# Optimization experiments

Hardware: AMD Instinct MI355X
Metric: run time of the kernel (lower is better)

Reference implementation:

```python
import jax, jax.numpy as jnp
import numpy as np

N = 50000      # nodes per type
E = 200000     # edges per relation
H, D = 4, 64   # heads, per-head dim
C = H * D      # hidden = hc_graph * heads = 256
L = 3          # num_hops (HGTConv layers)
HC_LIN, HC_TASK = 256, 128
OUT_DIMS = (3, 3, 3, 5, 1, 1, 8)  # ptr_l1/l2/l3, leaf_category, signed, floating, size


def setup_inputs() -> dict:
    key = jax.random.key(0)
    ks = jax.random.split(key, 24)
    f = lambda k, s: jax.random.normal(k, s, dtype=jnp.float32) * 0.05
    ri = lambda k: jax.random.randint(k, (E,), 0, N, dtype=jnp.int32)
    return {
        "xe": f(ks[0], (N, C)),
        "xs": f(ks[1], (N, C)),
        "ee_src": ri(ks[2]), "ee_dst": ri(ks[3]),
        "es_src": ri(ks[4]), "es_dst": ri(ks[5]),
        "se_src": ri(ks[6]), "se_dst": ri(ks[7]),
        # per-layer, per-node-type projections (2 node types)
        "Wk": f(ks[8], (L, 2, C, C)),
        "Wq": f(ks[9], (L, 2, C, C)),
        "Wv": f(ks[10], (L, 2, C, C)),
        "Wa": f(ks[11], (L, 2, C, C)),
        "skip": jnp.ones((L, 2), dtype=jnp.float32),
        # per-layer, per-relation attention/message transforms (3 relations)
        "Arel": f(ks[12], (L, 3, H, D, D)),
        "Mrel": f(ks[13], (L, 3, H, D, D)),
        "mu": jnp.ones((L, 3, H), dtype=jnp.float32),
        # shared linear stack + 7 task heads (final out padded to 8, sliced per head)
        "Wsh": f(ks[14], (2, HC_LIN, HC_LIN)),
        "bsh": jnp.zeros((2, HC_LIN), dtype=jnp.float32),
        "Wt1": f(ks[15], (7, HC_LIN, HC_TASK)),
        "bt1": jnp.zeros((7, HC_TASK), dtype=jnp.float32),
        "Wt2": f(ks[16], (7, HC_TASK, 8)),
        "bt2": jnp.zeros((7, 8), dtype=jnp.float32),
    }


def _seg_softmax(scores, seg, n):
    m = jax.ops.segment_max(scores, seg, num_segments=n)
    e = jnp.exp(scores - m[seg])
    s = jax.ops.segment_sum(e, seg, num_segments=n)
    return e / (s[seg] + 1e-16)


def _hgt_forward(xe, xs, ee_src, ee_dst, es_src, es_dst, se_src, se_dst,
                 Wk, Wq, Wv, Wa, skip, Arel, Mrel, mu, Wsh, bsh, Wt1, bt1, Wt2, bt2):
    inv_sqrt_d = 1.0 / jnp.sqrt(jnp.float32(D))

    def rel(k_src, v_src, q_dst, src, dst, A, M, m):
        kt = jnp.einsum('ehd,hdf->ehf', k_src[src], A)          # [E,H,D]
        score = (q_dst[dst] * kt).sum(-1) * (m * inv_sqrt_d)    # [E,H]
        msg = jnp.einsum('ehd,hdf->ehf', v_src[src], M)         # [E,H,D]
        return score, msg

    for l in range(L):
        ke = (xe @ Wk[l, 0]).reshape(N, H, D)
        qe = (xe @ Wq[l, 0]).reshape(N, H, D)
        ve = (xe @ Wv[l, 0]).reshape(N, H, D)
        ks_ = (xs @ Wk[l, 1]).reshape(N, H, D)
        qs = (xs @ Wq[l, 1]).reshape(N, H, D)
        vs = (xs @ Wv[l, 1]).reshape(N, H, D)

        s0, m0 = rel(ke, ve, qe, ee_src, ee_dst, Arel[l, 0], Mrel[l, 0], mu[l, 0])  # expr->expr
        s1, m1 = rel(ke, ve, qs, es_src, es_dst, Arel[l, 1], Mrel[l, 1], mu[l, 1])  # expr->stmt
        s2, m2 = rel(ks_, vs, qe, se_src, se_dst, Arel[l, 2], Mrel[l, 2], mu[l, 2])  # stmt->expr

        # destination 'expr': softmax over all incoming edges (rel0 + rel2)
        sc_e = jnp.concatenate([s0, s2], axis=0)
        ms_e = jnp.concatenate([m0, m2], axis=0)
        dst_e = jnp.concatenate([ee_dst, se_dst], axis=0)
        a_e = _seg_softmax(sc_e, dst_e, N)
        agg_e = jax.ops.segment_sum(a_e[..., None] * ms_e, dst_e, num_segments=N).reshape(N, C)

        # destination 'stmt': only rel1
        a_s = _seg_softmax(s1, es_dst, N)
        agg_s = jax.ops.segment_sum(a_s[..., None] * m1, es_dst, num_segments=N).reshape(N, C)

        be = jax.nn.sigmoid(skip[l, 0])
        bs = jax.nn.sigmoid(skip[l, 1])
        xe = be * (jax.nn.gelu(agg_e, approximate=False) @ Wa[l, 0]) + (1.0 - be) * xe
        xs = bs * (jax.nn.gelu(agg_s, approximate=False) @ Wa[l, 1]) + (1.0 - bs) * xs

    # shared linear stack on 'expr' nodes
    h = xe
    for i in range(Wsh.shape[0]):
        h = jax.nn.relu(h @ Wsh[i] + bsh[i])

    # 7 task heads: hidden layer + final (padded to 8 outputs, sliced per head)
    t = jax.nn.relu(jnp.einsum('nc,kct->knt', h, Wt1) + bt1[:, None, :])  # [7,N,HC_TASK]
    o = jnp.einsum('knt,kto->kno', t, Wt2) + bt2[:, None, :]              # [7,N,8]
    outs = [o[i, :, :d] for i, d in enumerate(OUT_DIMS)]
    return jnp.concatenate(outs, axis=-1)  # [N, 24]


def reference(xe, xs, ee_src, ee_dst, es_src, es_dst, se_src, se_dst,
              Wk, Wq, Wv, Wa, skip, Arel, Mrel, mu, Wsh, bsh, Wt1, bt1, Wt2, bt2):
    return _hgt_forward(xe, xs, ee_src, ee_dst, es_src, es_dst, se_src, se_dst,
                        Wk, Wq, Wv, Wa, skip, Arel, Mrel, mu, Wsh, bsh, Wt1, bt1, Wt2, bt2)
```

## Files before the change

### kernel.cpp

```cpp
#include <hip/hip_runtime.h>
#include <hip/hip_fp16.h>
#include <cmath>


#define CDIM 256
#define AR_R (256 * 256)

using f16x8 = __attribute__((ext_vector_type(8))) _Float16;
using f16x4 = __attribute__((ext_vector_type(4))) _Float16;
using f16x2 = __attribute__((ext_vector_type(2))) _Float16;
using f32x4 = __attribute__((ext_vector_type(4))) float;

__device__ __forceinline__ float gelu_f(float x) {
    return 0.5f * x * (1.0f + erff(x * 0.70710678118654752f));
}

__device__ __forceinline__ float dot8f(const f16x8 a, const f16x8 b, float r) {
#if __has_builtin(__builtin_amdgcn_fdot2)
#pragma unroll
    for (int t = 0; t < 4; ++t) {
        f16x2 av = {a[2 * t], a[2 * t + 1]};
        f16x2 bv = {b[2 * t], b[2 * t + 1]};
        r = __builtin_amdgcn_fdot2(av, bv, r, false);
    }
#else
#pragma unroll
    for (int t = 0; t < 8; ++t) r += (float)a[t] * (float)b[t];
#endif
    return r;
}

__global__ __launch_bounds__(256) void zero_k(int* __restrict__ p, size_t n) {
    size_t i = (size_t)blockIdx.x * blockDim.x + threadIdx.x;
    const size_t stride = (size_t)gridDim.x * blockDim.x;
    for (; i < n; i += stride) p[i] = 0;
}

__global__ __launch_bounds__(256) void cvt2_k(const float* __restrict__ xe_in,
                                              const float* __restrict__ xs_in,
                                              _Float16* __restrict__ xeH,
                                              _Float16* __restrict__ xsH,
                                              size_t n4) {
    const float* in = blockIdx.y ? xs_in : xe_in;
    _Float16* out = blockIdx.y ? xsH : xeH;
    size_t i = (size_t)blockIdx.x * blockDim.x + threadIdx.x;
    const size_t stride = (size_t)gridDim.x * blockDim.x;
    for (; i < n4; i += stride) {
        const float4 v = ((const float4*)in)[i];
        f16x4 o;
        o[0] = (_Float16)v.x; o[1] = (_Float16)v.y;
        o[2] = (_Float16)v.z; o[3] = (_Float16)v.w;
        ((f16x4*)out)[i] = o;
    }
}

__device__ __forceinline__ void cvtT_dev(const float* __restrict__ W,
                                         _Float16* __restrict__ dst) {
    const int o = blockIdx.x, c = threadIdx.x;
    dst[(size_t)o * 256 + c] = (_Float16)W[(size_t)c * 256 + o];
}

__device__ __forceinline__ void foldT_dev(const float* __restrict__ Wbase,
                                          const float* __restrict__ T,
                                          _Float16* __restrict__ dst) {
    __shared__ float row[256];
    const int c = blockIdx.x, t = threadIdx.x;
    row[t] = Wbase[(size_t)c * 256 + t];
    __syncthreads();
    const int h = t >> 6, f = t & 63;
    const float* Th = T + h * 4096;
    float acc = 0.f;
#pragma unroll 8
    for (int d = 0; d < 64; ++d) acc += row[h * 64 + d] * Th[d * 64 + f];
    dst[(size_t)t * 256 + c] = (_Float16)acc;
}

__global__ __launch_bounds__(256) void prep_layer_k(
    const float* __restrict__ Wk, const float* __restrict__ Wq,
    const float* __restrict__ Wv, const float* __restrict__ Wa,
    const float* __restrict__ Arel, const float* __restrict__ Mrel,
    _Float16* __restrict__ arena) {
    const size_t CC = 65536, HDD = 16384;
    const int l = blockIdx.y / 10;
    const int c = blockIdx.y % 10;
    _Float16* L = arena + (size_t)l * 10 * AR_R;
    const float* Wk0 = Wk + (l * 2 + 0) * CC;
    const float* Wk1 = Wk + (l * 2 + 1) * CC;
    const float* Wv0 = Wv + (l * 2 + 0) * CC;
    const float* Wv1 = Wv + (l * 2 + 1) * CC;
    switch (c) {
        case 0: cvtT_dev(Wq + (l * 2 + 0) * CC, L); break;
        case 1: foldT_dev(Wk0, Arel + (l * 3 + 0) * HDD, L + 1 * AR_R); break;
        case 2: foldT_dev(Wk0, Arel + (l * 3 + 1) * HDD, L + 2 * AR_R); break;
        case 3: cvtT_dev(Wq + (l * 2 + 1) * CC, L + 3 * AR_R); break;
        case 4: foldT_dev(Wk1, Arel + (l * 3 + 2) * HDD, L + 4 * AR_R); break;
        case 5: foldT_dev(Wv0, Mrel + (l * 3 + 0) * HDD, L + 5 * AR_R); break;
        case 6: foldT_dev(Wv0, Mrel + (l * 3 + 1) * HDD, L + 6 * AR_R); break;
        case 7: foldT_dev(Wv1, Mrel + (l * 3 + 2) * HDD, L + 7 * AR_R); break;
        case 8: cvtT_dev(Wa + (l * 2 + 0) * CC, L + 8 * AR_R); break;
        case 9: cvtT_dev(Wa + (l * 2 + 1) * CC, L + 9 * AR_R); break;
    }
}

__global__ __launch_bounds__(256) void prep_stack_k(const float* __restrict__ Wsh,
                                                    _Float16* __restrict__ SA) {
    cvtT_dev(Wsh + (size_t)blockIdx.y * 65536, SA + (size_t)blockIdx.y * AR_R);
}

__global__ __launch_bounds__(256) void prep_heads_k(const float* __restrict__ Wt1,
                                                    _Float16* __restrict__ HA) {
    const int o = blockIdx.x, k = blockIdx.y, c = threadIdx.x;
    HA[(size_t)(k * 128 + o) * 256 + c] =
        (_Float16)Wt1[(size_t)k * 256 * 128 + (size_t)c * 128 + o];
}

template <int EPI, bool SPLIT>
__device__ __forceinline__ void gemm_body(
    const _Float16* __restrict__ A, const _Float16* __restrict__ Bt,
    _Float16* __restrict__ C, int M, int Nc, int bm, int bn, size_t bufStride,
    const float* __restrict__ bias, const float* __restrict__ skipv,
    _Float16* As, _Float16* Bs) {
    const int tid = threadIdx.x;
    const int wave = tid >> 6, lane = tid & 63;
    const int wm = (wave >> 1) * 64, wn = (wave & 1) * 64;
    const int l15 = lane & 15, g = lane >> 4;

    f32x4 acc[4][4] = {};

    for (int k0 = 0; k0 < 256; k0 += 64) {
        __syncthreads();
#pragma unroll
        for (int p = 0; p < 4; ++p) {
            const int slot = p * 256 + tid;
            const int r = slot >> 3;
            const int cb = ((slot & 7) << 4) ^ ((r & 7) << 4);
            int gr = bm + r; if (gr >= M) gr = M - 1;
            __builtin_amdgcn_global_load_lds(
                (const __attribute__((address_space(1))) void*)
                    ((const char*)A + ((size_t)gr * 256 + k0) * 2 + cb),
                (__attribute__((address_space(3))) void*)((char*)As + slot * 16),
                16, 0, 0);
            __builtin_amdgcn_global_load_lds(
                (const __attribute__((address_space(1))) void*)
                    ((const char*)Bt + ((size_t)(bn + r) * 256 + k0) * 2 + cb),
                (__attribute__((address_space(3))) void*)((char*)Bs + slot * 16),
                16, 0, 0);
        }
        __syncthreads();
#pragma unroll
        for (int sub = 0; sub < 2; ++sub) {
            f16x8 af[4], bf[4];
#pragma unroll
            for (int i = 0; i < 4; ++i) {
                const int ra = wm + i * 16 + l15;
                const int rb = wn + i * 16 + l15;
                const int ka = (sub * 64 + g * 16) ^ ((ra & 7) << 4);
                const int kb = (sub * 64 + g * 16) ^ ((rb & 7) << 4);
                af[i] = *(const f16x8*)((const char*)As + ra * 128 + ka);
                bf[i] = *(const f16x8*)((const char*)Bs + rb * 128 + kb);
            }
#pragma unroll
            for (int mi = 0; mi < 4; ++mi)
#pragma unroll
                for (int ni = 0; ni < 4; ++ni)
                    acc[mi][ni] = __builtin_amdgcn_mfma_f32_16x16x32_f16(
                        af[mi], bf[ni], acc[mi][ni], 0, 0, 0);
        }
    }

    float be = 0.f, ombe = 0.f;
    if (EPI == 1) {
        const float s = skipv[0];
        be = 1.0f / (1.0f + expf(-s));
        ombe = 1.0f - be;
    }
#pragma unroll
    for (int mi = 0; mi < 4; ++mi) {
#pragma unroll
        for (int r = 0; r < 4; ++r) {
            const int row = bm + wm + mi * 16 + g * 4 + r;
            if (row >= M) continue;
#pragma unroll
            for (int ni = 0; ni < 4; ++ni) {
                const int colg = bn + wn + ni * 16 + l15;
                float v = acc[mi][ni][r];
                size_t idx;
                if (SPLIT)
                    idx = (size_t)(colg >> 8) * bufStride + (size_t)row * 256 +
                          (colg & 255);
                else
                    idx = (size_t)row * Nc + colg;
                if (EPI == 1) v = be * v + ombe * (float)C[idx];
                if (EPI == 2) v = fmaxf(v + bias[colg], 0.f);
                C[idx] = (_Float16)v;
            }
        }
    }
}

template <int EPI, bool SPLIT>
__global__ __launch_bounds__(256) void gemm_h(
    const _Float16* __restrict__ A, const _Float16* __restrict__ Bt,
    _Float16* __restrict__ C, int M, int Nc, size_t bufStride,
    const float* __restrict__ bias, const float* __restrict__ skipv) {
    __shared__ _Float16 As[128 * 64];
    __shared__ _Float16 Bs[128 * 64];
    gemm_body<EPI, SPLIT>(A, Bt, C, M, Nc, blockIdx.y * 128, blockIdx.x * 128,
                          bufStride, bias, skipv, As, Bs);
}

__global__ __launch_bounds__(256) void projq_k(
    const _Float16* __restrict__ xeH, const _Float16* __restrict__ xsH,
    const _Float16* __restrict__ L, _Float16* __restrict__ Hb, int M) {
    __shared__ _Float16 As[128 * 64];
    __shared__ _Float16 Bs[128 * 64];
    const int job = blockIdx.x >> 1;
    const int bn = (blockIdx.x & 1) * 128;
    const _Float16* A = (job < 3) ? xeH : xsH;
    const _Float16* Bt = L + (size_t)job * AR_R;
    _Float16* C = Hb + (size_t)job * (size_t)M * 256;
    gemm_body<0, false>(A, Bt, C, M, 256, blockIdx.y * 128, bn, 0, nullptr,
                        nullptr, As, Bs);
}

__global__ __launch_bounds__(256) void projv_k(
    const _Float16* __restrict__ xeH, const _Float16* __restrict__ xsH,
    const _Float16* __restrict__ L, _Float16* __restrict__ Hb, int M) {
    __shared__ _Float16 As[128 * 64];
    __shared__ _Float16 Bs[128 * 64];
    const int job = blockIdx.x >> 1;
    const int bn = (blockIdx.x & 1) * 128;
    const _Float16* A = (job < 2) ? xeH : xsH;
    const _Float16* Bt = L + (size_t)(5 + job) * AR_R;
    const int dsti = (job == 0) ? 1 : (job == 1) ? 2 : 4;
    _Float16* C = Hb + (size_t)dsti * (size_t)M * 256;
    gemm_body<0, false>(A, Bt, C, M, 256, blockIdx.y * 128, bn, 0, nullptr,
                        nullptr, As, Bs);
}

__global__ __launch_bounds__(256) void update2_k(
    const _Float16* __restrict__ aggE, const _Float16* __restrict__ aggS,
    const _Float16* __restrict__ WaT0, const _Float16* __restrict__ WaT1,
    _Float16* __restrict__ xeH, _Float16* __restrict__ xsH,
    const float* __restrict__ skipb, int M) {
    __shared__ _Float16 As[128 * 64];
    __shared__ _Float16 Bs[128 * 64];
    const int sel = blockIdx.x >> 1;
    const int bn = (blockIdx.x & 1) * 128;
    const int bm = blockIdx.y * 128;
    if (sel == 0)
        gemm_body<1, false>(aggE, WaT0, xeH, M, 256, bm, bn, 0, nullptr, skipb,
                            As, Bs);
    else
        gemm_body<1, false>(aggS, WaT1, xsH, M, 256, bm, bn, 0, nullptr,
                            skipb + 1, As, Bs);
}

__global__ __launch_bounds__(256) void hist3_k(const int* __restrict__ d0,
                                               const int* __restrict__ d1,
                                               const int* __restrict__ d2,
                                               int* __restrict__ cnt, int N,
                                               int E) {
    const int i = blockIdx.x * 256 + threadIdx.x;
    if (i >= E) return;
    const int r = blockIdx.y;
    const int* d = r == 0 ? d0 : r == 1 ? d1 : d2;
    atomicAdd(&cnt[(size_t)r * N + d[i]], 1);
}

__global__ __launch_bounds__(256) void partial_k(const int* __restrict__ cnt,
                                                 int* __restrict__ partials,
                                                 int N, int PB) {
    const int r = blockIdx.y, b = blockIdx.x, tid = threadIdx.x;
    const int gi = b * 256 + tid;
    int v = (gi < N) ? cnt[(size_t)r * N + gi] : 0;
#pragma unroll
    for (int o = 1; o < 64; o <<= 1) v += __shfl_xor(v, o);
    __shared__ int ws[4];
    if ((tid & 63) == 0) ws[tid >> 6] = v;
    __syncthreads();
    if (tid == 0) partials[r * PB + b] = ws[0] + ws[1] + ws[2] + ws[3];
}

__global__ __launch_bounds__(256) void scanp_k(int* __restrict__ partials,
                                               int* __restrict__ rp, int N,
                                               int PB, int E) {
    __shared__ int lds[256];
    const int r = blockIdx.y, tid = threadIdx.x;
    const int v = (tid < PB) ? partials[r * PB + tid] : 0;
    lds[tid] = v;
    __syncthreads();
    int acc = v;
    for (int off = 1; off < 256; off <<= 1) {
        const int t = (tid >= off) ? lds[tid - off] : 0;
        __syncthreads();
        acc += t;
        lds[tid] = acc;
        __syncthreads();
    }
    if (tid < PB) partials[r * PB + tid] = acc - v;
    if (tid == 0) rp[(size_t)r * (N + 1) + N] = E;
}

__global__ __launch_bounds__(256) void rpwrite_k(const int* __restrict__ cnt,
                                                 const int* __restrict__ partials,
                                                 int* __restrict__ rp, int N,
                                                 int PB) {
    __shared__ int lds[256];
    const int r = blockIdx.y, b = blockIdx.x, tid = threadIdx.x;
    const int gi = b * 256 + tid;
    const int v = (gi < N) ? cnt[(size_t)r * N + gi] : 0;
    lds[tid] = v;
    __syncthreads();
    int acc = v;
    for (int off = 1; off < 256; off <<= 1) {
        const int t = (tid >= off) ? lds[tid - off] : 0;
        __syncthreads();
        acc += t;
        lds[tid] = acc;
        __syncthreads();
    }
    if (gi < N) rp[(size_t)r * (N + 1) + gi] = partials[r * PB + b] + acc - v;
}

__global__ __launch_bounds__(256) void scatter3_k(
    const int* __restrict__ d0, const int* __restrict__ d1,
    const int* __restrict__ d2, const int* __restrict__ s0_,
    const int* __restrict__ s1_, const int* __restrict__ s2_,
    const int* __restrict__ rp, int* __restrict__ fill,
    int* __restrict__ colsrc, int N, int E) {
    const int i = blockIdx.x * 256 + threadIdx.x;
    if (i >= E) return;
    const int r = blockIdx.y;
    const int* d = r == 0 ? d0 : r == 1 ? d1 : d2;
    const int* s = r == 0 ? s0_ : r == 1 ? s1_ : s2_;
    const int dd = d[i];
    const int p = rp[(size_t)r * (N + 1) + dd] + atomicAdd(&fill[(size_t)r * N + dd], 1);
    colsrc[(size_t)r * E + p] = s[i];
}

__device__ __forceinline__ void score_rel_g(
    const f16x8 q0, const f16x8 q1, const _Float16* __restrict__ kA,
    const int* __restrict__ cs, int beg, int end, float scl,
    float* __restrict__ sc, int grp, int j, float& m) {
    int i = beg + grp;
    for (; i + 4 < end; i += 8) {
        const int sA = cs[i], sB = cs[i + 4];
        const _Float16* rowA = &kA[(size_t)sA * 256 + j * 16];
        const _Float16* rowB = &kA[(size_t)sB * 256 + j * 16];
        const f16x8 a0 = *(const f16x8*)rowA;
        const f16x8 a1 = *(const f16x8*)(rowA + 8);
        const f16x8 b0 = *(const f16x8*)rowB;
        const f16x8 b1 = *(const f16x8*)(rowB + 8);
        float p0 = dot8f(q1, a1, dot8f(q0, a0, 0.f));
        float p1 = dot8f(q1, b1, dot8f(q0, b0, 0.f));
        p0 += __shfl_xor(p0, 1); p1 += __shfl_xor(p1, 1);
        p0 += __shfl_xor(p0, 2); p1 += __shfl_xor(p1, 2);
        const float v0 = p0 * scl, v1 = p1 * scl;
        if ((j & 3) == 0) {
            sc[(size_t)i * 4 + (j >> 2)] = v0;
            sc[(size_t)(i + 4) * 4 + (j >> 2)] = v1;
            m = fmaxf(m, fmaxf(v0, v1));
        }
    }
    if (i < end) {
        const int sA = cs[i];
        const _Float16* row = &kA[(size_t)sA * 256 + j * 16];
        const f16x8 k0 = *(const f16x8*)row;
        const f16x8 k1 = *(const f16x8*)(row + 8);
        float p = dot8f(q1, k1, dot8f(q0, k0, 0.f));
        p += __shfl_xor(p, 1);
        p += __shfl_xor(p, 2);
        const float v = p * scl;
        if ((j & 3) == 0) {
            sc[(size_t)i * 4 + (j >> 2)] = v;
            m = fmaxf(m, v);
        }
    }
}

__global__ __launch_bounds__(256) void score3_k(
    const _Float16* __restrict__ qe, const _Float16* __restrict__ kA0,
    const _Float16* __restrict__ kA1, const _Float16* __restrict__ qs,
    const _Float16* __restrict__ kA2, const int* __restrict__ rp,
    const int* __restrict__ colsrc, const float* __restrict__ muL,
    float* __restrict__ sc, float* __restrict__ mx_e,
    float* __restrict__ mx_s, int N, int E) {
    const int wid = (blockIdx.x * blockDim.x + threadIdx.x) >> 6;
    if (wid >= N) return;
    const int lane = threadIdx.x & 63;
    const int grp = lane >> 4, j = lane & 15, h = j >> 2;
    const size_t E4 = (size_t)E * 4;
    float m = -1e30f;
    if (blockIdx.y == 0) {
        const _Float16* qrow = &qe[(size_t)wid * 256 + j * 16];
        const f16x8 q0 = *(const f16x8*)qrow;
        const f16x8 q1 = *(const f16x8*)(qrow + 8);
        score_rel_g(q0, q1, kA0, colsrc, rp[wid], rp[wid + 1],
                    muL[0 * 4 + h] * 0.125f, sc, grp, j, m);
        const int* rp2 = rp + 2 * (N + 1);
        score_rel_g(q0, q1, kA2, colsrc + 2 * (size_t)E, rp2[wid], rp2[wid + 1],
                    muL[2 * 4 + h] * 0.125f, sc + 2 * E4, grp, j, m);
        m = fmaxf(m, __shfl_xor(m, 16));
        m = fmaxf(m, __shfl_xor(m, 32));
        if (grp == 0 && (j & 3) == 0) mx_e[(size_t)wid * 4 + h] = m;
    } else {
        const _Float16* qrow = &qs[(size_t)wid * 256 + j * 16];
        const f16x8 q0 = *(const f16x8*)qrow;
        const f16x8 q1 = *(const f16x8*)(qrow + 8);
        const int* rp1 = rp + (N + 1);
        score_rel_g(q0, q1, kA1, colsrc + (size_t)E, rp1[wid], rp1[wid + 1],
                    muL[1 * 4 + h] * 0.125f, sc + E4, grp, j, m);
        m = fmaxf(m, __shfl_xor(m, 16));
        m = fmaxf(m, __shfl_xor(m, 32));
        if (grp == 0 && (j & 3) == 0) mx_s[(size_t)wid * 4 + h] = m;
    }
}

__device__ __forceinline__ void agg_rel_on(
    const float* __restrict__ sc, const _Float16* __restrict__ vM,
    const int* __restrict__ cs, int beg, int end, float mh, int grp, int j,
    int h, float* accf, float& den) {
    for (int i = beg + grp; i < end; i += 4) {
        const int s = cs[i];
        const float w = __expf(sc[(size_t)i * 4 + h] - mh);
        den += w;
        const _Float16* row = &vM[(size_t)s * 256 + j * 16];
        const f16x8 v0 = *(const f16x8*)row;
        const f16x8 v1 = *(const f16x8*)(row + 8);
#pragma unroll
        for (int t = 0; t < 8; ++t) accf[t] += w * (float)v0[t];
#pragma unroll
        for (int t = 0; t < 8; ++t) accf[8 + t] += w * (float)v1[t];
    }
}

__global__ __launch_bounds__(256) void agg3_k(
    const float* __restrict__ sc, const _Float16* __restrict__ vM0,
    const _Float16* __restrict__ vM1, const _Float16* __restrict__ vM2,
    const int* __restrict__ rp, const int* __restrict__ colsrc,
    const float* __restrict__ mx_e, const float* __restrict__ mx_s,
    _Float16* __restrict__ outE, _Float16* __restrict__ outS, int N, int E) {
    const int wid = (blockIdx.x * blockDim.x + threadIdx.x) >> 6;
    if (wid >= N) return;
    const int lane = threadIdx.x & 63;
    const int grp = lane >> 4, j = lane & 15, h = j >> 2;
    const size_t E4 = (size_t)E * 4;
    float accf[16] = {};
    float den = 0.f;
    _Float16* outp;
    if (blockIdx.y == 0) {
        const float mh = mx_e[(size_t)wid * 4 + h];
        const int b0 = rp[wid], e0 = rp[wid + 1];
        const int* rp2 = rp + 2 * (N + 1);
        const int b2 = rp2[wid], e2 = rp2[wid + 1];
        agg_rel_on(sc, vM0, colsrc, b0, e0, mh, grp, j, h, accf, den);
        agg_rel_on(sc + 2 * E4, vM2, colsrc + 2 * (size_t)E, b2, e2, mh, grp,
                   j, h, accf, den);
        outp = outE;
    } else {
        const float mh = mx_s[(size_t)wid * 4 + h];
        const int* rp1 = rp + (N + 1);
        const int b1 = rp1[wid], e1 = rp1[wid + 1];
        agg_rel_on(sc + E4, vM1, colsrc + (size_t)E, b1, e1, mh, grp, j, h,
                   accf, den);
        outp = outS;
    }
    den += __shfl_xor(den, 16);
    den += __shfl_xor(den, 32);
#pragma unroll
    for (int t = 0; t < 16; ++t) {
        accf[t] += __shfl_xor(accf[t], 16);
        accf[t] += __shfl_xor(accf[t], 32);
    }
    const float dinv = 1.0f / (den + 1e-16f);
    f16x4 o;
#pragma unroll
    for (int t = 0; t < 4; ++t)
        o[t] = (_Float16)gelu_f(accf[grp * 4 + t] * dinv);
    *(f16x4*)&outp[(size_t)wid * 256 + j * 16 + grp * 4] = o;
}

__global__ __launch_bounds__(256) void head2_k(const _Float16* __restrict__ t,
                                               const float* __restrict__ Wt2,
                                               const float* __restrict__ bt2,
                                               float* __restrict__ out, int M) {
    const int k = blockIdx.y;
    __shared__ float Ws[128 * 8];
    __shared__ float bs[8];
    const int tid = threadIdx.x;
    const float* W2 = Wt2 + (size_t)k * 1024;
    for (int i = tid; i < 1024; i += 256) Ws[i] = W2[i];
    if (tid < 8) bs[tid] = bt2[k * 8 + tid];
    __syncthreads();
    const int OFFA[7] = {0, 3, 6, 9, 14, 15, 16};
    const int DIMSA[7] = {3, 3, 3, 5, 1, 1, 8};
    const int nl = tid >> 3, o = tid & 7;
    const int n = blockIdx.x * 32 + nl;
    if (n >= M) return;
    const _Float16* tr = &t[(size_t)n * 896 + k * 128];
    float acc = bs[o];
#pragma unroll 8
    for (int d = 0; d < 128; ++d) acc += (float)tr[d] * Ws[d * 8 + o];
    if (o < DIMSA[k]) out[(size_t)n * 24 + OFFA[k] + o] = acc;
}


extern "C" void kernel_launch(void* const* d_in, const int* in_sizes, int n_in,
                              void* d_out, int out_size, void* d_ws,
                              size_t ws_size, hipStream_t stream) {
    const float* xe_in = (const float*)d_in[0];
    const float* xs_in = (const float*)d_in[1];
    const int* ee_src = (const int*)d_in[2];
    const int* ee_dst = (const int*)d_in[3];
    const int* es_src = (const int*)d_in[4];
    const int* es_dst = (const int*)d_in[5];
    const int* se_src = (const int*)d_in[6];
    const int* se_dst = (const int*)d_in[7];
    const float* Wk = (const float*)d_in[8];
    const float* Wq = (const float*)d_in[9];
    const float* Wv = (const float*)d_in[10];
    const float* Wa = (const float*)d_in[11];
    const float* skip = (const float*)d_in[12];
    const float* Arel = (const float*)d_in[13];
    const float* Mrel = (const float*)d_in[14];
    const float* mu = (const float*)d_in[15];
    const float* Wsh = (const float*)d_in[16];
    const float* bsh = (const float*)d_in[17];
    const float* Wt1 = (const float*)d_in[18];
    const float* bt1 = (const float*)d_in[19];
    const float* Wt2 = (const float*)d_in[20];
    const float* bt2 = (const float*)d_in[21];
    float* out = (float*)d_out;

    const int N = in_sizes[0] / CDIM;
    const int E = in_sizes[2];
    const size_t NC = (size_t)N * CDIM;
    const size_t E4 = (size_t)E * 4;
    const size_t N4 = (size_t)N * 4;
    const int PB = (N + 255) / 256;

    const size_t halfs = 7 * NC + 32 * (size_t)AR_R + 7 * 32768;
    const size_t floats = 3 * E4 + 2 * N4;
    const size_t ints =
        3 * (size_t)(N + 1) + 3 * (size_t)E + 3 * (size_t)N + 3 * (size_t)PB;
    const size_t need = halfs * 2 + floats * 4 + ints * 4;
    if (ws_size < need) return;

    _Float16* xeH = (_Float16*)d_ws;
    _Float16* xsH = xeH + NC;
    _Float16* Hb = xsH + NC;
    _Float16* H1 = Hb;
    _Float16* H2 = Hb + NC;
    _Float16* H3 = Hb + 2 * NC;
    _Float16* H4 = Hb + 3 * NC;
    _Float16* H5 = Hb + 4 * NC;
    _Float16* arena = Hb + 5 * NC;
    _Float16* SA = arena + (size_t)30 * AR_R;
    _Float16* HA = SA + (size_t)2 * AR_R;
    float* sc = (float*)(HA + (size_t)7 * 32768);
    float* mx_e = sc + 3 * E4;
    float* mx_s = mx_e + N4;
    int* rp = (int*)(mx_s + N4);
    int* colsrc = rp + 3 * (size_t)(N + 1);
    int* cnt = colsrc + 3 * (size_t)E;
    int* partials = cnt + 3 * (size_t)N;

    const int gx = (N + 127) / 128;
    const dim3 e3((E + 255) / 256, 3);
    const dim3 p3(PB, 3);
    const int wave_blocks = (N + 3) / 4;
    const int zc_blocks = (3 * N + 255) / 256;

    zero_k<<<zc_blocks, 256, 0, stream>>>(cnt, 3 * (size_t)N);
    hist3_k<<<e3, 256, 0, stream>>>(ee_dst, es_dst, se_dst, cnt, N, E);
    partial_k<<<p3, 256, 0, stream>>>(cnt, partials, N, PB);
    scanp_k<<<dim3(1, 3), 256, 0, stream>>>(partials, rp, N, PB, E);
    rpwrite_k<<<p3, 256, 0, stream>>>(cnt, partials, rp, N, PB);
    zero_k<<<zc_blocks, 256, 0, stream>>>(cnt, 3 * (size_t)N);
    scatter3_k<<<e3, 256, 0, stream>>>(ee_dst, es_dst, se_dst, ee_src, es_src,
                                       se_src, rp, cnt, colsrc, N, E);

    prep_layer_k<<<dim3(256, 30), 256, 0, stream>>>(Wk, Wq, Wv, Wa, Arel, Mrel,
                                                    arena);
    prep_stack_k<<<dim3(256, 2), 256, 0, stream>>>(Wsh, SA);
    prep_heads_k<<<dim3(128, 7), 256, 0, stream>>>(Wt1, HA);

    cvt2_k<<<dim3(1024, 2), 256, 0, stream>>>(xe_in, xs_in, xeH, xsH, NC / 4);

    for (int l = 0; l < 3; ++l) {
        _Float16* L = arena + (size_t)l * 10 * AR_R;
        projq_k<<<dim3(10, gx), 256, 0, stream>>>(xeH, xsH, L, Hb, N);
        score3_k<<<dim3(wave_blocks, 2), 256, 0, stream>>>(
            H1, H2, H3, H4, H5, rp, colsrc, mu + l * 12, sc, mx_e, mx_s, N, E);
        projv_k<<<dim3(6, gx), 256, 0, stream>>>(xeH, xsH, L, Hb, N);
        agg3_k<<<dim3(wave_blocks, 2), 256, 0, stream>>>(
            sc, H2, H3, H5, rp, colsrc, mx_e, mx_s, H1, H4, N, E);
        update2_k<<<dim3(4, gx), 256, 0, stream>>>(
            H1, H4, L + 8 * AR_R, L + 9 * AR_R, xeH, xsH, skip + l * 2, N);
    }

    gemm_h<2, false><<<dim3(2, gx), 256, 0, stream>>>(xeH, SA, H5, N, 256, 0,
                                                      bsh, nullptr);
    gemm_h<2, false><<<dim3(2, gx), 256, 0, stream>>>(H5, SA + AR_R, xsH, N,
                                                      256, 0, bsh + 256, nullptr);
    gemm_h<2, false><<<dim3(7, gx), 256, 0, stream>>>(xsH, HA, Hb, N, 896, 0,
                                                      bt1, nullptr);
    head2_k<<<dim3((N + 31) / 32, 7), 256, 0, stream>>>(Hb, Wt2, bt2, out, N);
}
```

Measured before the change: 1.044 ms.

## Schedule score and aggregation waves by descending node in-degree

Adds a counting sort of destination nodes by in-degree (clamped at 63), built once per call with a histogram, a suffix-offset pass and a scatter. The score and aggregation kernels then map each wave to a node through this order, so high-degree nodes launch first. The aim is to reduce tail imbalance from uneven per-node edge counts. In exchange, nodes processed next to each other are no longer contiguous in memory, which hurts locality of q/row-pointer/output accesses, and four small extra kernel launches are added.

```diff
diff --git a/kernel.cpp b/kernel.cpp
--- a/kernel.cpp
+++ b/kernel.cpp
@@ -339,6 +339,51 @@
     colsrc[(size_t)r * E + p] = s[i];
 }
 
+__global__ __launch_bounds__(256) void degh_k(const int* __restrict__ rp,
+                                              int* __restrict__ degk,
+                                              int* __restrict__ dhist, int N) {
+    __shared__ int lh[64];
+    const int dom = blockIdx.y, tid = threadIdx.x;
+    const int n = blockIdx.x * 256 + tid;
+    if (tid < 64) lh[tid] = 0;
+    __syncthreads();
+    if (n < N) {
+        int d;
+        if (dom == 0)
+            d = (rp[n + 1] - rp[n]) +
+                (rp[2 * (N + 1) + n + 1] - rp[2 * (N + 1) + n]);
+        else
+            d = rp[(N + 1) + n + 1] - rp[(N + 1) + n];
+        const int b = min(d, 63);
+        degk[(size_t)dom * N + n] = b;
+        atomicAdd(&lh[b], 1);
+    }
+    __syncthreads();
+    if (tid < 64 && lh[tid]) atomicAdd(&dhist[dom * 64 + tid], lh[tid]);
+}
+
+__global__ __launch_bounds__(128) void degoff_k(int* __restrict__ dhist) {
+    __shared__ int h[128];
+    const int tid = threadIdx.x;
+    h[tid] = dhist[tid];
+    __syncthreads();
+    const int dom = tid >> 6, b = tid & 63;
+    int off = 0;
+    for (int bb = b + 1; bb < 64; ++bb) off += h[dom * 64 + bb];
+    dhist[tid] = off;
+}
+
+__global__ __launch_bounds__(256) void degsc_k(const int* __restrict__ degk,
+                                               int* __restrict__ dhist,
+                                               int* __restrict__ order, int N) {
+    const int dom = blockIdx.y;
+    const int n = blockIdx.x * 256 + threadIdx.x;
+    if (n >= N) return;
+    const int b = degk[(size_t)dom * N + n];
+    const int p = atomicAdd(&dhist[dom * 64 + b], 1);
+    order[(size_t)dom * N + p] = n;
+}
+
 __device__ __forceinline__ void score_rel_g(
     const f16x8 q0, const f16x8 q1, const _Float16* __restrict__ kA,
     const int* __restrict__ cs, int beg, int end, float scl,
@@ -383,16 +428,18 @@
     const _Float16* __restrict__ qe, const _Float16* __restrict__ kA0,
     const _Float16* __restrict__ kA1, const _Float16* __restrict__ qs,
     const _Float16* __restrict__ kA2, const int* __restrict__ rp,
-    const int* __restrict__ colsrc, const float* __restrict__ muL,
-    float* __restrict__ sc, float* __restrict__ mx_e,
-    float* __restrict__ mx_s, int N, int E) {
-    const int wid = (blockIdx.x * blockDim.x + threadIdx.x) >> 6;
-    if (wid >= N) return;
+    const int* __restrict__ colsrc, const int* __restrict__ order,
+    const float* __restrict__ muL, float* __restrict__ sc,
+    float* __restrict__ mx_e, float* __restrict__ mx_s, int N, int E) {
+    const int widx = (blockIdx.x * blockDim.x + threadIdx.x) >> 6;
+    if (widx >= N) return;
     const int lane = threadIdx.x & 63;
     const int grp = lane >> 4, j = lane & 15, h = j >> 2;
     const size_t E4 = (size_t)E * 4;
+    const int dom = blockIdx.y;
+    const int wid = order[(size_t)dom * N + widx];
     float m = -1e30f;
-    if (blockIdx.y == 0) {
+    if (dom == 0) {
         const _Float16* qrow = &qe[(size_t)wid * 256 + j * 16];
         const f16x8 q0 = *(const f16x8*)qrow;
         const f16x8 q1 = *(const f16x8*)(qrow + 8);
@@ -439,17 +486,20 @@
     const float* __restrict__ sc, const _Float16* __restrict__ vM0,
     const _Float16* __restrict__ vM1, const _Float16* __restrict__ vM2,
     const int* __restrict__ rp, const int* __restrict__ colsrc,
-    const float* __restrict__ mx_e, const float* __restrict__ mx_s,
-    _Float16* __restrict__ outE, _Float16* __restrict__ outS, int N, int E) {
-    const int wid = (blockIdx.x * blockDim.x + threadIdx.x) >> 6;
-    if (wid >= N) return;
+    const int* __restrict__ order, const float* __restrict__ mx_e,
+    const float* __restrict__ mx_s, _Float16* __restrict__ outE,
+    _Float16* __restrict__ outS, int N, int E) {
+    const int widx = (blockIdx.x * blockDim.x + threadIdx.x) >> 6;
+    if (widx >= N) return;
     const int lane = threadIdx.x & 63;
     const int grp = lane >> 4, j = lane & 15, h = j >> 2;
     const size_t E4 = (size_t)E * 4;
+    const int dom = blockIdx.y;
+    const int wid = order[(size_t)dom * N + widx];
     float accf[16] = {};
     float den = 0.f;
     _Float16* outp;
-    if (blockIdx.y == 0) {
+    if (dom == 0) {
         const float mh = mx_e[(size_t)wid * 4 + h];
         const int b0 = rp[wid], e0 = rp[wid + 1];
         const int* rp2 = rp + 2 * (N + 1);
@@ -542,8 +592,8 @@
 
     const size_t halfs = 7 * NC + 32 * (size_t)AR_R + 7 * 32768;
     const size_t floats = 3 * E4 + 2 * N4;
-    const size_t ints =
-        3 * (size_t)(N + 1) + 3 * (size_t)E + 3 * (size_t)N + 3 * (size_t)PB;
+    const size_t ints = 3 * (size_t)(N + 1) + 3 * (size_t)E + 3 * (size_t)N +
+                        3 * (size_t)PB + 4 * (size_t)N + 128;
     const size_t need = halfs * 2 + floats * 4 + ints * 4;
     if (ws_size < need) return;
 
@@ -565,10 +615,14 @@
     int* colsrc = rp + 3 * (size_t)(N + 1);
     int* cnt = colsrc + 3 * (size_t)E;
     int* partials = cnt + 3 * (size_t)N;
+    int* degk = partials + 3 * (size_t)PB;
+    int* order = degk + 2 * (size_t)N;
+    int* dhist = order + 2 * (size_t)N;
 
     const int gx = (N + 127) / 128;
     const dim3 e3((E + 255) / 256, 3);
     const dim3 p3(PB, 3);
+    const dim3 n2((N + 255) / 256, 2);
     const int wave_blocks = (N + 3) / 4;
     const int zc_blocks = (3 * N + 255) / 256;
 
@@ -581,6 +635,11 @@
     scatter3_k<<<e3, 256, 0, stream>>>(ee_dst, es_dst, se_dst, ee_src, es_src,
                                        se_src, rp, cnt, colsrc, N, E);
 
+    zero_k<<<1, 128, 0, stream>>>(dhist, 128);
+    degh_k<<<n2, 256, 0, stream>>>(rp, degk, dhist, N);
+    degoff_k<<<1, 128, 0, stream>>>(dhist);
+    degsc_k<<<n2, 256, 0, stream>>>(degk, dhist, order, N);
+
     prep_layer_k<<<dim3(256, 30), 256, 0, stream>>>(Wk, Wq, Wv, Wa, Arel, Mrel,
                                                     arena);
     prep_stack_k<<<dim3(256, 2), 256, 0, stream>>>(Wsh, SA);
@@ -592,10 +651,11 @@
         _Float16* L = arena + (size_t)l * 10 * AR_R;
         projq_k<<<dim3(10, gx), 256, 0, stream>>>(xeH, xsH, L, Hb, N);
         score3_k<<<dim3(wave_blocks, 2), 256, 0, stream>>>(
-            H1, H2, H3, H4, H5, rp, colsrc, mu + l * 12, sc, mx_e, mx_s, N, E);
+            H1, H2, H3, H4, H5, rp, colsrc, order, mu + l * 12, sc, mx_e, mx_s,
+            N, E);
         projv_k<<<dim3(6, gx), 256, 0, stream>>>(xeH, xsH, L, Hb, N);
         agg3_k<<<dim3(wave_blocks, 2), 256, 0, stream>>>(
-            sc, H2, H3, H5, rp, colsrc, mx_e, mx_s, H1, H4, N, E);
+            sc, H2, H3, H5, rp, colsrc, order, mx_e, mx_s, H1, H4, N, E);
         update2_k<<<dim3(4, gx), 256, 0, stream>>>(
             H1, H4, L + 8 * AR_R, L + 9 * AR_R, xeH, xsH, skip + l * 2, N);
     }
```

Result: slower. 1.308 ms (+25.4%).
